# Optimization experiments

Hardware: AMD Instinct MI355X
Metric: run time of the kernel (lower is better)

## Reference

```python
import jax, jax.numpy as jnp
import numpy as np

N_WIRES = 16
N_LAYERS = 10


def _pairs(n):
    p = [(i, i + 1) for i in range(0, n - 1, 2)]
    if n > 2:
        p.append((n - 1, 0))
    return p


def _rot_u(tx, ty, tz):
    # Combined single-qubit rotation U = RZ(tz) @ RY(ty) @ RX(tx), shape [B,2,2] complex64.
    cx, sx = jnp.cos(0.5 * tx), jnp.sin(0.5 * tx)
    cy, sy = jnp.cos(0.5 * ty), jnp.sin(0.5 * ty)
    ez = jnp.exp(-1j * (0.5 * tz).astype(jnp.complex64))  # e^{-i tz/2}
    z = jnp.zeros_like(ez)
    RX = jnp.stack([jnp.stack([cx + 0j, -1j * sx], -1),
                    jnp.stack([-1j * sx, cx + 0j], -1)], -2)
    RY = jnp.stack([jnp.stack([cy + 0j, -sy + 0j], -1),
                    jnp.stack([sy + 0j, cy + 0j], -1)], -2)
    RZ = jnp.stack([jnp.stack([ez, z], -1),
                    jnp.stack([z, jnp.conj(ez)], -1)], -2)
    return jnp.einsum('bij,bjk,bkl->bil', RZ, RY, RX)


def _apply_1q(state, U, w):
    # state: [B, 2, 2, ..., 2] (n_wires axes after batch); wire w is axis w+1.
    s = jnp.moveaxis(state, w + 1, 1)
    s = jnp.einsum('bij,bj...->bi...', U, s)
    return jnp.moveaxis(s, 1, w + 1)


def _cnot(state, c, t):
    # Flip target axis t where control axis c is |1>.
    a0 = jax.lax.index_in_dim(state, 0, axis=c + 1, keepdims=True)
    a1 = jax.lax.index_in_dim(state, 1, axis=c + 1, keepdims=True)
    a1 = jnp.flip(a1, axis=t + 1)
    return jnp.concatenate([a0, a1], axis=c + 1)


def setup_inputs() -> dict:
    key = jax.random.key(0)
    params = jax.random.normal(key, (128, 3 * N_WIRES * N_LAYERS), dtype=jnp.float32)
    return {"params": params}


def reference(params):
    B = params.shape[0]
    n = N_WIRES
    state = jnp.zeros((B, 2 ** n), jnp.complex64).at[:, 0].set(1.0)
    state = state.reshape((B,) + (2,) * n)
    pairs = _pairs(n)
    for layer in range(N_LAYERS):
        for (c, t) in pairs:
            state = _cnot(state, c, t)
        base = layer * 3 * n
        for i in range(n):
            U = _rot_u(params[:, base + 3 * i + 0],
                       params[:, base + 3 * i + 1],
                       params[:, base + 3 * i + 2])
            state = _apply_1q(state, U, i)
    states = state.reshape(B, -1)
    return jnp.abs(states) ** 2
```

## Files before the change

### kernel.cpp

```cpp
#include <hip/hip_runtime.h>


#define NB 128
#define NL 10

__device__ __forceinline__ void getU(const float* __restrict__ p,
                                     float& u00r, float& u00i,
                                     float& u01r, float& u01i) {
    float sx, cx, sy, cy, sz, cz;
    sincosf(0.5f * p[0], &sx, &cx);
    sincosf(0.5f * p[1], &sy, &cy);
    sincosf(0.5f * p[2], &sz, &cz);
    u00r =  cz * cy * cx + sz * sy * sx;
    u00i =  cz * sy * sx - sz * cy * cx;
    u01r = -cz * sy * cx - sz * cy * sx;
    u01i = -cz * cy * sx + sz * sy * cx;
}

__global__ __launch_bounds__(256, 8) void vqc_fused(const float* __restrict__ params,
                                                    float* __restrict__ out) {
    const int bb = blockIdx.x >> 2;
    const int q  = blockIdx.x & 3;
    const int t  = threadIdx.x;

    __shared__ float4 Us[NL * 16];
    __shared__ float  p4s[16];
    __shared__ float  p2s[6][4];
    __shared__ float  g[64];
    __shared__ float  fi_s[16];

    if (t < NL * 16) {
        const int L = t >> 4, w = t & 15;
        const float* p = params + bb * (48 * NL) + L * 48 + w * 3;
        float a, b, c, d;
        getU(p, a, b, c, d);
        Us[t] = make_float4(a, b, c, d);
    }
    __syncthreads();

    if (t < 64) {
        const bool isC0   = (t < 16);
        const bool isPair = (t >= 16 && t < 40);
        const int  k      = isPair ? ((t - 16) >> 2) : 0;
        const int  lb     = isC0 ? t : (t & 3);
        int p1 = t, p2 = t, p3 = t;
        if (isC0) {
            p1 = t ^ ((t & 8) >> 1);
            p2 = t ^ ((t & 2) >> 1);
            p3 = t ^ ((t & 1) << 3);
        } else if (isPair) {
            p1 = (t & ~3) | (lb ^ ((lb & 2) >> 1));
        }
        int m4 = 0, m5 = 0, m6 = 0, m7 = 0;
        int w4 = 0, w5 = 0, w6 = 0, w7 = 0;
        if (isC0)      { m4 = 8; w4 = 0;          m5 = 4; w5 = 1;
                         m6 = 2; w6 = 14;         m7 = 1; w7 = 15; }
        else if (isPair) { m4 = 2; w4 = 2 * k + 2; m5 = 1; w5 = 2 * k + 3; }

        float vr = (lb == 0 && (isC0 || isPair)) ? 1.f : 0.f;
        float vi = 0.f;

#define PERM(SRC)                         \
    do {                                  \
        vr = __shfl(vr, (SRC), 64);       \
        vi = __shfl(vi, (SRC), 64);       \
    } while (0)
#define ROT(M, W)                                                   \
    do {                                                            \
        const int m_ = (M);                                         \
        float4 U = Us[L * 16 + (W)];                                \
        float prr = __shfl(vr, t ^ m_, 64);                         \
        float pri = __shfl(vi, t ^ m_, 64);                         \
        const bool act = m_ != 0;                                   \
        const bool up  = (lb & m_) == 0;                            \
        float cor = act ? U.x : 1.f;                                \
        float coi = act ? (up ? U.y : -U.y) : 0.f;                  \
        float cpr = act ? (up ? U.z : -U.z) : 0.f;                  \
        float cpi = act ? U.w : 0.f;                                \
        float nr = cor * vr - coi * vi + cpr * prr - cpi * pri;     \
        float ni = cor * vi + coi * vr + cpr * pri + cpi * prr;     \
        vr = nr;                                                    \
        vi = ni;                                                    \
    } while (0)

#pragma unroll 1
        for (int L = 0; L < NL; ++L) {
            PERM(p1);
            PERM(p2);
            PERM(p3);
            ROT(m4, w4);
            ROT(m5, w5);
            ROT(m6, w6);
            ROT(m7, w7);
        }
#undef PERM
#undef ROT
        const float pr = vr * vr + vi * vi;
        if (isC0) p4s[t] = pr;
        else if (isPair) p2s[k][lb] = pr;
    }
    __syncthreads();

    if (t < 64)
        g[t] = p2s[4][(t >> 4) & 3] * p2s[5][(t >> 2) & 3] *
               p4s[(q << 2) | (t & 3)];
    if (t < 16) fi_s[t] = p2s[0][t >> 2] * p2s[1][t & 3];
    __syncthreads();

    const float ft = p2s[2][t >> 6] * p2s[3][(t >> 4) & 3];
    const float4 g4 = *(const float4*)&g[(t & 15) << 2];
    const float g0 = ft * g4.x, g1 = ft * g4.y, g2 = ft * g4.z, g3 = ft * g4.w;
    float4* ob = (float4*)(out + (((size_t)bb << 16) | ((size_t)q << 14)));
#pragma unroll
    for (int i = 0; i < 16; ++i) {
        const float f = fi_s[i];
        ob[(i << 8) | t] = make_float4(f * g0, f * g1, f * g2, f * g3);
    }
}

extern "C" void kernel_launch(void* const* d_in, const int* in_sizes, int n_in,
                              void* d_out, int out_size, void* d_ws, size_t ws_size,
                              hipStream_t stream) {
    const float* params = (const float*)d_in[0];
    float* out = (float*)d_out;
    vqc_fused<<<512, 256, 0, stream>>>(params, out);
}
```

Measured before the change: 17.23 us.

## Split fused kernel into factor computation and output expansion kernels

Replaces the single fused kernel, which recomputed the per-batch state factors in each of four blocks per batch, with two kernels. The first computes the factor probabilities once per batch and stores them in workspace. The second expands them into the 2^16 outputs using 2048 lighter blocks. This removes redundant simulation work and spreads the store phase over more blocks, at the cost of an extra launch and a global round trip for the factors.

```diff
diff --git a/kernel.cpp b/kernel.cpp
--- a/kernel.cpp
+++ b/kernel.cpp
@@ -17,17 +17,12 @@
     u01i = -cz * cy * sx + sz * sy * cx;
 }
 
-__global__ __launch_bounds__(256, 8) void vqc_fused(const float* __restrict__ params,
-                                                    float* __restrict__ out) {
-    const int bb = blockIdx.x >> 2;
-    const int q  = blockIdx.x & 3;
+__global__ __launch_bounds__(256, 4) void factor_kernel(const float* __restrict__ params,
+                                                        float* __restrict__ fac) {
+    const int bb = blockIdx.x;
     const int t  = threadIdx.x;
 
     __shared__ float4 Us[NL * 16];
-    __shared__ float  p4s[16];
-    __shared__ float  p2s[6][4];
-    __shared__ float  g[64];
-    __shared__ float  fi_s[16];
 
     if (t < NL * 16) {
         const int L = t >> 4, w = t & 15;
@@ -53,9 +48,9 @@
         }
         int m4 = 0, m5 = 0, m6 = 0, m7 = 0;
         int w4 = 0, w5 = 0, w6 = 0, w7 = 0;
-        if (isC0)      { m4 = 8; w4 = 0;          m5 = 4; w5 = 1;
-                         m6 = 2; w6 = 14;         m7 = 1; w7 = 15; }
-        else if (isPair) { m4 = 2; w4 = 2 * k + 2; m5 = 1; w5 = 2 * k + 3; }
+        if (isC0)        { m4 = 8; w4 = 0;          m5 = 4; w5 = 1;
+                           m6 = 2; w6 = 14;         m7 = 1; w7 = 15; }
+        else if (isPair) { m4 = 2; w4 = 2 * k + 2;  m5 = 1; w5 = 2 * k + 3; }
 
         float vr = (lb == 0 && (isC0 || isPair)) ? 1.f : 0.f;
         float vi = 0.f;
@@ -96,25 +91,33 @@
 #undef PERM
 #undef ROT
         const float pr = vr * vr + vi * vi;
-        if (isC0) p4s[t] = pr;
-        else if (isPair) p2s[k][lb] = pr;
+        if (isC0)        fac[bb * 64 + t] = pr;
+        else if (isPair) fac[bb * 64 + 16 + k * 4 + lb] = pr;
     }
+}
+
+__global__ __launch_bounds__(256, 8) void expand_kernel(const float* __restrict__ fac,
+                                                        float* __restrict__ out) {
+    const int bb  = blockIdx.x >> 4;
+    const int nib = blockIdx.x & 15;
+    const int t   = threadIdx.x;
+
+    __shared__ float Lf[40];
+    if (t < 40) Lf[t] = fac[bb * 64 + t];
     __syncthreads();
 
-    if (t < 64)
-        g[t] = p2s[4][(t >> 4) & 3] * p2s[5][(t >> 2) & 3] *
-               p4s[(q << 2) | (t & 3)];
-    if (t < 16) fi_s[t] = p2s[0][t >> 2] * p2s[1][t & 3];
-    __syncthreads();
+    const float Ft = Lf[24 + (t >> 6)] * Lf[28 + ((t >> 4) & 3)] *
+                     Lf[32 + ((t >> 2) & 3)] * Lf[36 + (t & 3)];
+    const int p4b = (nib >> 2) << 2;
+    const float p40 = Lf[p4b + 0], p41 = Lf[p4b + 1];
+    const float p42 = Lf[p4b + 2], p43 = Lf[p4b + 3];
+    const float f0 = Lf[16 + (nib & 3)] * Ft;
 
-    const float ft = p2s[2][t >> 6] * p2s[3][(t >> 4) & 3];
-    const float4 g4 = *(const float4*)&g[(t & 15) << 2];
-    const float g0 = ft * g4.x, g1 = ft * g4.y, g2 = ft * g4.z, g3 = ft * g4.w;
-    float4* ob = (float4*)(out + (((size_t)bb << 16) | ((size_t)q << 14)));
+    float4* ob = (float4*)out + (((size_t)bb << 14) | ((size_t)nib << 10));
 #pragma unroll
-    for (int i = 0; i < 16; ++i) {
-        const float f = fi_s[i];
-        ob[(i << 8) | t] = make_float4(f * g0, f * g1, f * g2, f * g3);
+    for (int e = 0; e < 4; ++e) {
+        const float fe = f0 * Lf[20 + e];
+        ob[(e << 8) | t] = make_float4(fe * p40, fe * p41, fe * p42, fe * p43);
     }
 }
 
@@ -123,5 +126,8 @@
                               hipStream_t stream) {
     const float* params = (const float*)d_in[0];
     float* out = (float*)d_out;
-    vqc_fused<<<512, 256, 0, stream>>>(params, out);
+    float* fac = (float*)d_ws;
+
+    factor_kernel<<<NB, 256, 0, stream>>>(params, fac);
+    expand_kernel<<<2048, 256, 0, stream>>>(fac, out);
 }
```

Result: slower. 18.40 us (+6.7%).

## Compose CNOT shuffles into one permutation, unroll layers, split output across more blocks

Applied to the files above, without the earlier changes.

Merges the three per-layer CNOT shuffle permutations into a single precomputed source lane, cutting the shuffle count from six to two per layer. Fully unrolls the layer loop. Grid doubles to 1024 blocks, each writing an eighth of a batch's output. The output factorisation drops the intermediate shared arrays and the second barrier by computing products directly in registers. More blocks means the simulation prologue is repeated redundantly, in exchange for more parallelism on the store-bound output phase.

```diff
diff --git a/kernel.cpp b/kernel.cpp
--- a/kernel.cpp
+++ b/kernel.cpp
@@ -19,15 +19,13 @@
 
 __global__ __launch_bounds__(256, 8) void vqc_fused(const float* __restrict__ params,
                                                     float* __restrict__ out) {
-    const int bb = blockIdx.x >> 2;
-    const int q  = blockIdx.x & 3;
-    const int t  = threadIdx.x;
+    const int bb  = blockIdx.x >> 3;
+    const int oct = blockIdx.x & 7;
+    const int t   = threadIdx.x;
 
     __shared__ float4 Us[NL * 16];
     __shared__ float  p4s[16];
     __shared__ float  p2s[6][4];
-    __shared__ float  g[64];
-    __shared__ float  fi_s[16];
 
     if (t < NL * 16) {
         const int L = t >> 4, w = t & 15;
@@ -43,28 +41,23 @@
         const bool isPair = (t >= 16 && t < 40);
         const int  k      = isPair ? ((t - 16) >> 2) : 0;
         const int  lb     = isC0 ? t : (t & 3);
-        int p1 = t, p2 = t, p3 = t;
+        int sg = t;
         if (isC0) {
-            p1 = t ^ ((t & 8) >> 1);
-            p2 = t ^ ((t & 2) >> 1);
-            p3 = t ^ ((t & 1) << 3);
+            int u = t ^ ((t & 1) << 3);
+            int w = u ^ ((u & 2) >> 1);
+            sg    = w ^ ((w & 8) >> 1);
         } else if (isPair) {
-            p1 = (t & ~3) | (lb ^ ((lb & 2) >> 1));
+            sg = (t & ~3) | (lb ^ ((lb & 2) >> 1));
         }
         int m4 = 0, m5 = 0, m6 = 0, m7 = 0;
         int w4 = 0, w5 = 0, w6 = 0, w7 = 0;
-        if (isC0)      { m4 = 8; w4 = 0;          m5 = 4; w5 = 1;
-                         m6 = 2; w6 = 14;         m7 = 1; w7 = 15; }
-        else if (isPair) { m4 = 2; w4 = 2 * k + 2; m5 = 1; w5 = 2 * k + 3; }
+        if (isC0)        { m4 = 8; w4 = 0;          m5 = 4; w5 = 1;
+                           m6 = 2; w6 = 14;         m7 = 1; w7 = 15; }
+        else if (isPair) { m4 = 2; w4 = 2 * k + 2;  m5 = 1; w5 = 2 * k + 3; }
 
         float vr = (lb == 0 && (isC0 || isPair)) ? 1.f : 0.f;
         float vi = 0.f;
 
-#define PERM(SRC)                         \
-    do {                                  \
-        vr = __shfl(vr, (SRC), 64);       \
-        vi = __shfl(vi, (SRC), 64);       \
-    } while (0)
 #define ROT(M, W)                                                   \
     do {                                                            \
         const int m_ = (M);                                         \
@@ -83,38 +76,33 @@
         vi = ni;                                                    \
     } while (0)
 
-#pragma unroll 1
+#pragma unroll
         for (int L = 0; L < NL; ++L) {
-            PERM(p1);
-            PERM(p2);
-            PERM(p3);
+            vr = __shfl(vr, sg, 64);
+            vi = __shfl(vi, sg, 64);
             ROT(m4, w4);
             ROT(m5, w5);
             ROT(m6, w6);
             ROT(m7, w7);
         }
-#undef PERM
 #undef ROT
         const float pr = vr * vr + vi * vi;
-        if (isC0) p4s[t] = pr;
+        if (isC0)        p4s[t] = pr;
         else if (isPair) p2s[k][lb] = pr;
     }
     __syncthreads();
 
-    if (t < 64)
-        g[t] = p2s[4][(t >> 4) & 3] * p2s[5][(t >> 2) & 3] *
-               p4s[(q << 2) | (t & 3)];
-    if (t < 16) fi_s[t] = p2s[0][t >> 2] * p2s[1][t & 3];
-    __syncthreads();
+    const float Ft = p2s[2][t >> 6] * p2s[3][(t >> 4) & 3] *
+                     p2s[4][(t >> 2) & 3] * p2s[5][t & 3];
+    const int p4b = (oct >> 1) << 2;
+    const float p40 = p4s[p4b + 0], p41 = p4s[p4b + 1];
+    const float p42 = p4s[p4b + 2], p43 = p4s[p4b + 3];
 
-    const float ft = p2s[2][t >> 6] * p2s[3][(t >> 4) & 3];
-    const float4 g4 = *(const float4*)&g[(t & 15) << 2];
-    const float g0 = ft * g4.x, g1 = ft * g4.y, g2 = ft * g4.z, g3 = ft * g4.w;
-    float4* ob = (float4*)(out + (((size_t)bb << 16) | ((size_t)q << 14)));
+    float4* ob = (float4*)out + (((size_t)bb << 14) | ((size_t)oct << 11));
 #pragma unroll
-    for (int i = 0; i < 16; ++i) {
-        const float f = fi_s[i];
-        ob[(i << 8) | t] = make_float4(f * g0, f * g1, f * g2, f * g3);
+    for (int i = 0; i < 8; ++i) {
+        const float fe = Ft * p2s[0][((oct & 1) << 1) | (i >> 2)] * p2s[1][i & 3];
+        ob[(i << 8) | t] = make_float4(fe * p40, fe * p41, fe * p42, fe * p43);
     }
 }
 
@@ -123,5 +111,5 @@
                               hipStream_t stream) {
     const float* params = (const float*)d_in[0];
     float* out = (float*)d_out;
-    vqc_fused<<<512, 256, 0, stream>>>(params, out);
+    vqc_fused<<<1024, 256, 0, stream>>>(params, out);
 }
```

After: 15.52 us. 9.9% less time.
